# Kernel optimization log

Hardware: AMD Instinct MI355X
Metric: run time of the kernel (lower is better)

## Reference

```python
import jax, jax.numpy as jnp
import numpy as np


def setup_inputs() -> dict:
    B, I, H = 4096, 512, 1024
    key = jax.random.key(0)
    ks = jax.random.split(key, 10)
    return {
        "input": jax.random.normal(ks[0], (B, I), dtype=jnp.float32),
        "t": jax.random.uniform(ks[1], (B, 1), dtype=jnp.float32),
        "hx": jax.random.normal(ks[2], (B, H), dtype=jnp.float32),
        "cx": jax.random.normal(ks[3], (B, H), dtype=jnp.float32),
        "weight_ih": jax.random.normal(ks[4], (4 * H, I), dtype=jnp.float32),
        "weight_hh": jax.random.normal(ks[5], (4 * H, H), dtype=jnp.float32),
        "bias_ih": jax.random.normal(ks[6], (4 * H,), dtype=jnp.float32),
        "bias_hh": jax.random.normal(ks[7], (4 * H,), dtype=jnp.float32),
        "W_decomp": jax.random.normal(ks[8], (H, H), dtype=jnp.float32),
        "b_decomp": jax.random.normal(ks[9], (H,), dtype=jnp.float32),
    }


def reference(input, t, hx, cx, weight_ih, weight_hh, bias_ih, bias_hh, W_decomp, b_decomp):
    H = W_decomp.shape[0]
    # gates: [B, 4H]
    gates = input @ weight_ih.T + bias_ih + hx @ weight_hh.T + bias_hh
    ingate, forgetgate, cellgate, outgate = jnp.split(gates, 4, axis=1)
    # time-decay factor g(t): elementwise 1/t where t != 0, broadcast [B,1] -> [B,H]
    T = jnp.where(t != 0, 1.0 / jnp.where(t != 0, t, 1.0), 0.0)  # [B, 1]
    T = jnp.broadcast_to(T, (t.shape[0], H))
    # T-LSTM cell-state decomposition
    C_ST = jnp.tanh(cx @ W_decomp + b_decomp)
    cx_adj = cx - C_ST + T * C_ST
    ingate = jax.nn.sigmoid(ingate)
    forgetgate = jax.nn.sigmoid(forgetgate)
    cellgate = jnp.tanh(cellgate)
    outgate = jax.nn.sigmoid(outgate)
    cy = forgetgate * cx_adj + ingate * cellgate
    hy = outgate * jnp.tanh(cy)
    return (hy, cy)
```

## Files before the change

### kernel.cpp

```cpp
#include <hip/hip_runtime.h>
#include <cstdint>


typedef __attribute__((ext_vector_type(8))) __bf16 bf16x8;
typedef __attribute__((ext_vector_type(4))) float f32x4;

__device__ __forceinline__ unsigned short f2bf_rn(float f) {
  unsigned int u = __float_as_uint(f);
  unsigned int r = u + 0x7fffu + ((u >> 16) & 1u);
  return (unsigned short)(r >> 16);
}
__device__ __forceinline__ float bf2f(unsigned short h) {
  return __uint_as_float(((unsigned int)h) << 16);
}
__device__ __forceinline__ float sigm_f(float x) {
  return 1.0f / (1.0f + __expf(-x));
}
__device__ __forceinline__ float tanh_f(float x) {
  return 1.0f - 2.0f / (__expf(2.0f * x) + 1.0f);
}
__device__ __forceinline__ void gl_lds16(const void* g, void* l) {
  __builtin_amdgcn_global_load_lds(
      (const __attribute__((address_space(1))) void*)g,
      (__attribute__((address_space(3))) void*)l, 16, 0, 0);
}

__global__ __launch_bounds__(384) void prep_k(
    const float* __restrict__ input, const float* __restrict__ hx,
    const float* __restrict__ w_ih, const float* __restrict__ w_hh,
    const float* __restrict__ cx,
    unsigned short* __restrict__ Xhi, unsigned short* __restrict__ Xlo,
    unsigned short* __restrict__ Whi, unsigned short* __restrict__ Wlo,
    unsigned short* __restrict__ Chi, unsigned short* __restrict__ Clo) {
  const int bid = blockIdx.x;
  const int k = threadIdx.x << 2;
  const float* src;
  unsigned short *hi, *lo;
  if (bid < 4096) {
    const long m = bid;
    src = (k < 512) ? (input + m * 512 + k) : (hx + m * 1024 + (k - 512));
    hi = Xhi + m * 1536 + k;
    lo = Xlo + m * 1536 + k;
  } else if (bid < 8192) {
    const int n = bid - 4096;
    const int g = n >> 10;
    const int h = n & 1023;
    const long nd = ((long)(h >> 4) << 6) | (g << 4) | (h & 15);
    src = (k < 512) ? (w_ih + (long)n * 512 + k) : (w_hh + (long)n * 1024 + (k - 512));
    hi = Whi + nd * 1536 + k;
    lo = Wlo + nd * 1536 + k;
  } else {
    if (k >= 1024) return;
    const long m = bid - 8192;
    src = cx + m * 1024 + k;
    hi = Chi + m * 1024 + k;
    lo = Clo + m * 1024 + k;
  }
  float4 v = *(const float4*)src;
  ushort4 hv, lv;
  hv.x = f2bf_rn(v.x); lv.x = f2bf_rn(v.x - bf2f(hv.x));
  hv.y = f2bf_rn(v.y); lv.y = f2bf_rn(v.y - bf2f(hv.y));
  hv.z = f2bf_rn(v.z); lv.z = f2bf_rn(v.z - bf2f(hv.z));
  hv.w = f2bf_rn(v.w); lv.w = f2bf_rn(v.w - bf2f(hv.w));
  *(ushort4*)hi = hv;
  *(ushort4*)lo = lv;
}

__global__ void transpose_split_k(const float* __restrict__ W, int Ndim,
                                  unsigned short* __restrict__ Thi,
                                  unsigned short* __restrict__ Tlo) {
  __shared__ float tile[64][65];
  const int bx = blockIdx.x * 64;
  const int by = blockIdx.y * 64;
  const int tx = threadIdx.x;
  for (int r = threadIdx.y; r < 64; r += 4)
    tile[r][tx] = W[(long)(by + r) * Ndim + bx + tx];
  __syncthreads();
  for (int r = threadIdx.y; r < 64; r += 4) {
    float v = tile[tx][r];
    unsigned short h = f2bf_rn(v);
    long o = (long)(bx + r) * Ndim + by + tx;
    Thi[o] = h;
    Tlo[o] = f2bf_rn(v - bf2f(h));
  }
}

__global__ __launch_bounds__(512, 2) void gemm_mega(
    const unsigned short* __restrict__ Xh, const unsigned short* __restrict__ Xl,
    const unsigned short* __restrict__ Wh, const unsigned short* __restrict__ Wl,
    const unsigned short* __restrict__ Ch, const unsigned short* __restrict__ Cl,
    const unsigned short* __restrict__ Dh, const unsigned short* __restrict__ Dl,
    const float* __restrict__ b_ih, const float* __restrict__ b_hh,
    const float* __restrict__ b_d, const float* __restrict__ cx,
    const float* __restrict__ t, float* __restrict__ out) {
  __shared__ __align__(16) unsigned short sAh[2][8192];
  __shared__ __align__(16) unsigned short sAl[2][8192];
  __shared__ __align__(16) unsigned short sBh[2][4096];
  __shared__ __align__(16) unsigned short sBl[2][4096];

  const int swz = ((blockIdx.x & 7) << 6) | (blockIdx.x >> 3);
  const int n_blk = swz & 31;
  const int m_blk = swz >> 5;
  const int m0 = m_blk * 256;
  const int n0 = n_blk * 128;
  const int h0 = n_blk * 32;

  const int tid = threadIdx.x;
  const int wave = tid >> 6;
  const int lane = tid & 63;
  const int wr = wave >> 1;
  const int wc = wave & 1;
  const int srow = lane >> 2;
  const int ssw = (((lane & 3) ^ ((lane >> 3) & 3)) << 3);
  const int fm = lane & 15;
  const int fq = lane >> 4;
  const int psw = (fq ^ ((fm >> 1) & 3)) << 3;

#define STAGE1(B_, KT_)                                                        \
  {                                                                            \
    const long gA0 = (long)(m0 + wave * 32 + srow) * 1024 + (KT_) + ssw;       \
    gl_lds16(Ch + gA0, &sAh[B_][(wave * 32) * 32]);                            \
    gl_lds16(Cl + gA0, &sAl[B_][(wave * 32) * 32]);                            \
    const long gA1 = gA0 + 16 * 1024;                                          \
    gl_lds16(Ch + gA1, &sAh[B_][(wave * 32 + 16) * 32]);                       \
    gl_lds16(Cl + gA1, &sAl[B_][(wave * 32 + 16) * 32]);                       \
    if (wave < 4) {                                                            \
      const int rb = (wave & 1) * 16;                                          \
      const long gD = (long)(h0 + rb + srow) * 1024 + (KT_) + ssw;             \
      if (wave & 2) gl_lds16(Dl + gD, &sBl[B_][rb * 32]);                      \
      else          gl_lds16(Dh + gD, &sBh[B_][rb * 32]);                      \
    }                                                                          \
  }

#define STAGE2(B_, KT_)                                                        \
  {                                                                            \
    const long gA0 = (long)(m0 + wave * 32 + srow) * 1536 + (KT_) + ssw;       \
    gl_lds16(Xh + gA0, &sAh[B_][(wave * 32) * 32]);                            \
    gl_lds16(Xl + gA0, &sAl[B_][(wave * 32) * 32]);                            \
    const long gA1 = gA0 + 16 * 1536;                                          \
    gl_lds16(Xh + gA1, &sAh[B_][(wave * 32 + 16) * 32]);                       \
    gl_lds16(Xl + gA1, &sAl[B_][(wave * 32 + 16) * 32]);                       \
    const long gB0 = (long)(n0 + wave * 16 + srow) * 1536 + (KT_) + ssw;       \
    gl_lds16(Wh + gB0, &sBh[B_][(wave * 16) * 32]);                            \
    gl_lds16(Wl + gB0, &sBl[B_][(wave * 16) * 32]);                            \
  }

  f32x4 dacc[4];
#pragma unroll
  for (int i = 0; i < 4; ++i) dacc[i] = {0.f, 0.f, 0.f, 0.f};

  STAGE1(0, 0);
#pragma unroll 2
  for (int it = 0; it < 32; ++it) {
    const int b = it & 1;
    if (it < 31) {
      STAGE1(b ^ 1, (it + 1) * 32);
      if (wave < 4) asm volatile("s_waitcnt vmcnt(5)" ::: "memory");
      else          asm volatile("s_waitcnt vmcnt(4)" ::: "memory");
    } else {
      asm volatile("s_waitcnt vmcnt(0)" ::: "memory");
    }
    __builtin_amdgcn_s_barrier();
    bf16x8 ah[4], al[4];
#pragma unroll
    for (int mf = 0; mf < 4; ++mf) {
      const int ao = (wr * 64 + mf * 16 + fm) * 32 + psw;
      ah[mf] = *(const bf16x8*)&sAh[b][ao];
      al[mf] = *(const bf16x8*)&sAl[b][ao];
    }
    const int bo = (wc * 16 + fm) * 32 + psw;
    const bf16x8 bh = *(const bf16x8*)&sBh[b][bo];
    const bf16x8 bl = *(const bf16x8*)&sBl[b][bo];
    __builtin_amdgcn_s_setprio(1);
#pragma unroll
    for (int mf = 0; mf < 4; ++mf) {
      dacc[mf] = __builtin_amdgcn_mfma_f32_16x16x32_bf16(ah[mf], bh, dacc[mf], 0, 0, 0);
      dacc[mf] = __builtin_amdgcn_mfma_f32_16x16x32_bf16(ah[mf], bl, dacc[mf], 0, 0, 0);
      dacc[mf] = __builtin_amdgcn_mfma_f32_16x16x32_bf16(al[mf], bh, dacc[mf], 0, 0, 0);
    }
    __builtin_amdgcn_s_setprio(0);
    __builtin_amdgcn_s_barrier();
  }

  f32x4 acc[4][4];
#pragma unroll
  for (int i = 0; i < 4; ++i)
#pragma unroll
    for (int j = 0; j < 4; ++j) acc[i][j] = {0.f, 0.f, 0.f, 0.f};

  STAGE2(0, 0);
#pragma unroll 2
  for (int it = 0; it < 48; ++it) {
    const int b = it & 1;
    if (it < 47) {
      STAGE2(b ^ 1, (it + 1) * 32);
      asm volatile("s_waitcnt vmcnt(6)" ::: "memory");
    } else {
      asm volatile("s_waitcnt vmcnt(0)" ::: "memory");
    }
    __builtin_amdgcn_s_barrier();
    bf16x8 ah[4], al[4], bh[4], bl[4];
#pragma unroll
    for (int mf = 0; mf < 4; ++mf) {
      const int ao = (wr * 64 + mf * 16 + fm) * 32 + psw;
      ah[mf] = *(const bf16x8*)&sAh[b][ao];
      al[mf] = *(const bf16x8*)&sAl[b][ao];
    }
#pragma unroll
    for (int nf = 0; nf < 4; ++nf) {
      const int bo = (wc * 64 + nf * 16 + fm) * 32 + psw;
      bh[nf] = *(const bf16x8*)&sBh[b][bo];
      bl[nf] = *(const bf16x8*)&sBl[b][bo];
    }
    __builtin_amdgcn_s_setprio(1);
#pragma unroll
    for (int nf = 0; nf < 4; ++nf)
#pragma unroll
      for (int mf = 0; mf < 4; ++mf) {
        acc[mf][nf] = __builtin_amdgcn_mfma_f32_16x16x32_bf16(ah[mf], bh[nf], acc[mf][nf], 0, 0, 0);
        acc[mf][nf] = __builtin_amdgcn_mfma_f32_16x16x32_bf16(ah[mf], bl[nf], acc[mf][nf], 0, 0, 0);
        acc[mf][nf] = __builtin_amdgcn_mfma_f32_16x16x32_bf16(al[mf], bh[nf], acc[mf][nf], 0, 0, 0);
      }
    __builtin_amdgcn_s_setprio(0);
    __builtin_amdgcn_s_barrier();
  }

  const int h = h0 + wc * 16 + fm;
  const float bi  = b_ih[h]        + b_hh[h];
  const float bff = b_ih[1024 + h] + b_hh[1024 + h];
  const float bg  = b_ih[2048 + h] + b_hh[2048 + h];
  const float bo2 = b_ih[3072 + h] + b_hh[3072 + h];
  const float bd  = b_d[h];
#pragma unroll
  for (int mf = 0; mf < 4; ++mf) {
#pragma unroll
    for (int r = 0; r < 4; ++r) {
      const int m = m0 + wr * 64 + mf * 16 + fq * 4 + r;
      const float tv = t[m];
      const float T = (tv != 0.0f) ? (1.0f / tv) : 0.0f;
      const float cst = tanh_f(dacc[mf][r] + bd);
      const float cadj = cx[(long)m * 1024 + h] + (T - 1.0f) * cst;
      const float ig = sigm_f(acc[mf][0][r] + bi);
      const float fg = sigm_f(acc[mf][1][r] + bff);
      const float cg = tanh_f(acc[mf][2][r] + bg);
      const float og = sigm_f(acc[mf][3][r] + bo2);
      const float cyv = fg * cadj + ig * cg;
      const float hyv = og * tanh_f(cyv);
      out[(long)m * 1024 + h] = hyv;
      out[4096L * 1024 + (long)m * 1024 + h] = cyv;
    }
  }
#undef STAGE1
#undef STAGE2
}

extern "C" void kernel_launch(void* const* d_in, const int* in_sizes, int n_in,
                              void* d_out, int out_size, void* d_ws, size_t ws_size,
                              hipStream_t stream) {
  const float* input = (const float*)d_in[0];
  const float* t     = (const float*)d_in[1];
  const float* hx    = (const float*)d_in[2];
  const float* cx    = (const float*)d_in[3];
  const float* w_ih  = (const float*)d_in[4];
  const float* w_hh  = (const float*)d_in[5];
  const float* b_ih  = (const float*)d_in[6];
  const float* b_hh  = (const float*)d_in[7];
  const float* Wd    = (const float*)d_in[8];
  const float* b_d   = (const float*)d_in[9];

  const long B = 4096, H = 1024, KX = 1536, NG = 4096;

  char* ws = (char*)d_ws;
  unsigned short* Xhi = (unsigned short*)ws; ws += B * KX * 2;
  unsigned short* Xlo = (unsigned short*)ws; ws += B * KX * 2;
  unsigned short* Whi = (unsigned short*)ws; ws += NG * KX * 2;
  unsigned short* Wlo = (unsigned short*)ws; ws += NG * KX * 2;
  unsigned short* Chi = (unsigned short*)ws; ws += B * H * 2;
  unsigned short* Clo = (unsigned short*)ws; ws += B * H * 2;
  unsigned short* Dhi = (unsigned short*)ws; ws += H * H * 2;
  unsigned short* Dlo = (unsigned short*)ws; ws += H * H * 2;

  prep_k<<<12288, 384, 0, stream>>>(input, hx, w_ih, w_hh, cx,
                                    Xhi, Xlo, Whi, Wlo, Chi, Clo);
  transpose_split_k<<<dim3(16, 16), dim3(64, 4), 0, stream>>>(Wd, 1024, Dhi, Dlo);
  gemm_mega<<<512, 512, 0, stream>>>(Xhi, Xlo, Whi, Wlo, Chi, Clo, Dhi, Dlo,
                                     b_ih, b_hh, b_d, cx, t, (float*)d_out);
}
```

Baseline: 360.0 us.

## Split MFMA inner loops into quadrant phases with interleaved LDS reads and barriers

Each K-step of both GEMM loops is split into several phases. Each phase loads only part of the A/B fragments from LDS, runs the MFMAs for one quadrant of the accumulator tile, and ends with a barrier. The aim is to stagger LDS reads against MFMA execution across waves, in a ping-pong style schedule. The cost is several extra s_barrier calls per iteration, which may add synchronisation stalls.

New measurement: 382.7 us. +6.3%, slower.

```diff
diff --git a/kernel.cpp b/kernel.cpp
--- a/kernel.cpp
+++ b/kernel.cpp
@@ -161,22 +161,38 @@
       asm volatile("s_waitcnt vmcnt(0)" ::: "memory");
     }
     __builtin_amdgcn_s_barrier();
-    bf16x8 ah[4], al[4];
-#pragma unroll
-    for (int mf = 0; mf < 4; ++mf) {
+    bf16x8 ah01[2], al01[2];
+#pragma unroll
+    for (int mf = 0; mf < 2; ++mf) {
       const int ao = (wr * 64 + mf * 16 + fm) * 32 + psw;
-      ah[mf] = *(const bf16x8*)&sAh[b][ao];
-      al[mf] = *(const bf16x8*)&sAl[b][ao];
+      ah01[mf] = *(const bf16x8*)&sAh[b][ao];
+      al01[mf] = *(const bf16x8*)&sAl[b][ao];
     }
     const int bo = (wc * 16 + fm) * 32 + psw;
     const bf16x8 bh = *(const bf16x8*)&sBh[b][bo];
     const bf16x8 bl = *(const bf16x8*)&sBl[b][bo];
     __builtin_amdgcn_s_setprio(1);
 #pragma unroll
-    for (int mf = 0; mf < 4; ++mf) {
-      dacc[mf] = __builtin_amdgcn_mfma_f32_16x16x32_bf16(ah[mf], bh, dacc[mf], 0, 0, 0);
-      dacc[mf] = __builtin_amdgcn_mfma_f32_16x16x32_bf16(ah[mf], bl, dacc[mf], 0, 0, 0);
-      dacc[mf] = __builtin_amdgcn_mfma_f32_16x16x32_bf16(al[mf], bh, dacc[mf], 0, 0, 0);
+    for (int mf = 0; mf < 2; ++mf) {
+      dacc[mf] = __builtin_amdgcn_mfma_f32_16x16x32_bf16(ah01[mf], bh, dacc[mf], 0, 0, 0);
+      dacc[mf] = __builtin_amdgcn_mfma_f32_16x16x32_bf16(ah01[mf], bl, dacc[mf], 0, 0, 0);
+      dacc[mf] = __builtin_amdgcn_mfma_f32_16x16x32_bf16(al01[mf], bh, dacc[mf], 0, 0, 0);
+    }
+    __builtin_amdgcn_s_setprio(0);
+    __builtin_amdgcn_s_barrier();
+    bf16x8 ah23[2], al23[2];
+#pragma unroll
+    for (int mf = 0; mf < 2; ++mf) {
+      const int ao = (wr * 64 + (mf + 2) * 16 + fm) * 32 + psw;
+      ah23[mf] = *(const bf16x8*)&sAh[b][ao];
+      al23[mf] = *(const bf16x8*)&sAl[b][ao];
+    }
+    __builtin_amdgcn_s_setprio(1);
+#pragma unroll
+    for (int mf = 0; mf < 2; ++mf) {
+      dacc[mf + 2] = __builtin_amdgcn_mfma_f32_16x16x32_bf16(ah23[mf], bh, dacc[mf + 2], 0, 0, 0);
+      dacc[mf + 2] = __builtin_amdgcn_mfma_f32_16x16x32_bf16(ah23[mf], bl, dacc[mf + 2], 0, 0, 0);
+      dacc[mf + 2] = __builtin_amdgcn_mfma_f32_16x16x32_bf16(al23[mf], bh, dacc[mf + 2], 0, 0, 0);
     }
     __builtin_amdgcn_s_setprio(0);
     __builtin_amdgcn_s_barrier();
@@ -199,27 +215,74 @@
       asm volatile("s_waitcnt vmcnt(0)" ::: "memory");
     }
     __builtin_amdgcn_s_barrier();
-    bf16x8 ah[4], al[4], bh[4], bl[4];
-#pragma unroll
-    for (int mf = 0; mf < 4; ++mf) {
+    bf16x8 ah01[2], al01[2], bh01[2], bl01[2];
+#pragma unroll
+    for (int mf = 0; mf < 2; ++mf) {
       const int ao = (wr * 64 + mf * 16 + fm) * 32 + psw;
-      ah[mf] = *(const bf16x8*)&sAh[b][ao];
-      al[mf] = *(const bf16x8*)&sAl[b][ao];
-    }
-#pragma unroll
-    for (int nf = 0; nf < 4; ++nf) {
+      ah01[mf] = *(const bf16x8*)&sAh[b][ao];
+      al01[mf] = *(const bf16x8*)&sAl[b][ao];
+    }
+#pragma unroll
+    for (int nf = 0; nf < 2; ++nf) {
       const int bo = (wc * 64 + nf * 16 + fm) * 32 + psw;
-      bh[nf] = *(const bf16x8*)&sBh[b][bo];
-      bl[nf] = *(const bf16x8*)&sBl[b][bo];
-    }
-    __builtin_amdgcn_s_setprio(1);
-#pragma unroll
-    for (int nf = 0; nf < 4; ++nf)
-#pragma unroll
-      for (int mf = 0; mf < 4; ++mf) {
-        acc[mf][nf] = __builtin_amdgcn_mfma_f32_16x16x32_bf16(ah[mf], bh[nf], acc[mf][nf], 0, 0, 0);
-        acc[mf][nf] = __builtin_amdgcn_mfma_f32_16x16x32_bf16(ah[mf], bl[nf], acc[mf][nf], 0, 0, 0);
-        acc[mf][nf] = __builtin_amdgcn_mfma_f32_16x16x32_bf16(al[mf], bh[nf], acc[mf][nf], 0, 0, 0);
+      bh01[nf] = *(const bf16x8*)&sBh[b][bo];
+      bl01[nf] = *(const bf16x8*)&sBl[b][bo];
+    }
+    __builtin_amdgcn_s_setprio(1);
+#pragma unroll
+    for (int nf = 0; nf < 2; ++nf)
+#pragma unroll
+      for (int mf = 0; mf < 2; ++mf) {
+        acc[mf][nf] = __builtin_amdgcn_mfma_f32_16x16x32_bf16(ah01[mf], bh01[nf], acc[mf][nf], 0, 0, 0);
+        acc[mf][nf] = __builtin_amdgcn_mfma_f32_16x16x32_bf16(ah01[mf], bl01[nf], acc[mf][nf], 0, 0, 0);
+        acc[mf][nf] = __builtin_amdgcn_mfma_f32_16x16x32_bf16(al01[mf], bh01[nf], acc[mf][nf], 0, 0, 0);
+      }
+    __builtin_amdgcn_s_setprio(0);
+    __builtin_amdgcn_s_barrier();
+    bf16x8 bh23[2], bl23[2];
+#pragma unroll
+    for (int nf = 0; nf < 2; ++nf) {
+      const int bo = (wc * 64 + (nf + 2) * 16 + fm) * 32 + psw;
+      bh23[nf] = *(const bf16x8*)&sBh[b][bo];
+      bl23[nf] = *(const bf16x8*)&sBl[b][bo];
+    }
+    __builtin_amdgcn_s_setprio(1);
+#pragma unroll
+    for (int nf = 0; nf < 2; ++nf)
+#pragma unroll
+      for (int mf = 0; mf < 2; ++mf) {
+        acc[mf][nf + 2] = __builtin_amdgcn_mfma_f32_16x16x32_bf16(ah01[mf], bh23[nf], acc[mf][nf + 2], 0, 0, 0);
+        acc[mf][nf + 2] = __builtin_amdgcn_mfma_f32_16x16x32_bf16(ah01[mf], bl23[nf], acc[mf][nf + 2], 0, 0, 0);
+        acc[mf][nf + 2] = __builtin_amdgcn_mfma_f32_16x16x32_bf16(al01[mf], bh23[nf], acc[mf][nf + 2], 0, 0, 0);
+      }
+    __builtin_amdgcn_s_setprio(0);
+    __builtin_amdgcn_s_barrier();
+    bf16x8 ah23[2], al23[2];
+#pragma unroll
+    for (int mf = 0; mf < 2; ++mf) {
+      const int ao = (wr * 64 + (mf + 2) * 16 + fm) * 32 + psw;
+      ah23[mf] = *(const bf16x8*)&sAh[b][ao];
+      al23[mf] = *(const bf16x8*)&sAl[b][ao];
+    }
+    __builtin_amdgcn_s_setprio(1);
+#pragma unroll
+    for (int nf = 0; nf < 2; ++nf)
+#pragma unroll
+      for (int mf = 0; mf < 2; ++mf) {
+        acc[mf + 2][nf + 2] = __builtin_amdgcn_mfma_f32_16x16x32_bf16(ah23[mf], bh23[nf], acc[mf + 2][nf + 2], 0, 0, 0);
+        acc[mf + 2][nf + 2] = __builtin_amdgcn_mfma_f32_16x16x32_bf16(ah23[mf], bl23[nf], acc[mf + 2][nf + 2], 0, 0, 0);
+        acc[mf + 2][nf + 2] = __builtin_amdgcn_mfma_f32_16x16x32_bf16(al23[mf], bh23[nf], acc[mf + 2][nf + 2], 0, 0, 0);
+      }
+    __builtin_amdgcn_s_setprio(0);
+    __builtin_amdgcn_s_barrier();
+    __builtin_amdgcn_s_setprio(1);
+#pragma unroll
+    for (int nf = 0; nf < 2; ++nf)
+#pragma unroll
+      for (int mf = 0; mf < 2; ++mf) {
+        acc[mf + 2][nf] = __builtin_amdgcn_mfma_f32_16x16x32_bf16(ah23[mf], bh01[nf], acc[mf + 2][nf], 0, 0, 0);
+        acc[mf + 2][nf] = __builtin_amdgcn_mfma_f32_16x16x32_bf16(ah23[mf], bl01[nf], acc[mf + 2][nf], 0, 0, 0);
+        acc[mf + 2][nf] = __builtin_amdgcn_mfma_f32_16x16x32_bf16(al23[mf], bh01[nf], acc[mf + 2][nf], 0, 0, 0);
       }
     __builtin_amdgcn_s_setprio(0);
     __builtin_amdgcn_s_barrier();
```
